# Optimization experiments

Measured on AMD Instinct MI355X. Metric: run time of the kernel, lower is better.

Reference implementation:

```python
import jax, jax.numpy as jnp
import numpy as np

N_NODES = 50000
N_EDGES = 800000
N_GRAPHS = 8
BN_EPS = 1e-5


def setup_inputs() -> dict:
    key = jax.random.key(0)
    ks = iter(jax.random.split(key, 40))
    d = {}
    d["x"] = jax.random.normal(next(ks), (N_NODES, 3), dtype=jnp.float32)
    d["edge_index"] = jax.random.randint(next(ks), (2, N_EDGES), 0, N_NODES, dtype=jnp.int32)
    d["batch"] = jnp.sort(jax.random.randint(next(ks), (N_NODES,), 0, N_GRAPHS, dtype=jnp.int32))
    conv_in = [3, 64, 128]  # dense concat widths feeding each GCN layer
    for i, cin in enumerate(conv_in):
        d[f"W{i}"] = jax.random.normal(next(ks), (cin, 64), dtype=jnp.float32) * (1.0 / np.sqrt(cin))
        d[f"b{i}"] = jax.random.normal(next(ks), (64,), dtype=jnp.float32) * 0.05
        d[f"g{i}"] = jax.random.uniform(next(ks), (64,), dtype=jnp.float32) + 0.5
        d[f"beta{i}"] = jax.random.normal(next(ks), (64,), dtype=jnp.float32) * 0.05
        d[f"rm{i}"] = jax.random.normal(next(ks), (64,), dtype=jnp.float32) * 0.05
        d[f"rv{i}"] = jax.random.uniform(next(ks), (64,), dtype=jnp.float32) + 0.5
    def lin(k, i, o):
        return (jax.random.normal(k, (i, o), dtype=jnp.float32) * (1.0 / np.sqrt(i)),)
    d["enc_w0"], = lin(next(ks), 256, 128); d["enc_b0"] = jax.random.normal(next(ks), (128,), jnp.float32) * 0.05
    d["enc_w1"], = lin(next(ks), 128, 64); d["enc_b1"] = jax.random.normal(next(ks), (64,), jnp.float32) * 0.05
    d["dec_w0"], = lin(next(ks), 64, 32); d["dec_b0"] = jax.random.normal(next(ks), (32,), jnp.float32) * 0.05
    d["dec_w1"], = lin(next(ks), 32, 1); d["dec_b1"] = jax.random.normal(next(ks), (1,), jnp.float32) * 0.05
    return d


def reference(x, edge_index, batch,
              W0, b0, g0, beta0, rm0, rv0,
              W1, b1, g1, beta1, rm1, rv1,
              W2, b2, g2, beta2, rm2, rv2,
              enc_w0, enc_b0, enc_w1, enc_b1,
              dec_w0, dec_b0, dec_w1, dec_b1):
    N = x.shape[0]
    loops = jnp.arange(N, dtype=edge_index.dtype)
    src = jnp.concatenate([edge_index[0], loops])  # GCNConv adds self loops
    dst = jnp.concatenate([edge_index[1], loops])
    deg = jax.ops.segment_sum(jnp.ones_like(src, dtype=x.dtype), dst, num_segments=N)
    dinv = jnp.where(deg > 0, jax.lax.rsqrt(deg), 0.0)
    coef = (dinv[src] * dinv[dst])[:, None]  # symmetric normalization per edge

    def conv_bn_relu(h, W, b, g, beta, rm, rv):
        hw = h @ W                                    # [N, 64]
        out = jax.ops.segment_sum(hw[src] * coef, dst, num_segments=N) + b
        out = (out - rm) * (g * jax.lax.rsqrt(rv + BN_EPS)) + beta  # BN eval mode
        return jax.nn.relu(out)

    params = [(W0, b0, g0, beta0, rm0, rv0),
              (W1, b1, g1, beta1, rm1, rv1),
              (W2, b2, g2, beta2, rm2, rv2)]
    prev = []
    h = x
    for p in params:  # dense connectivity: concat all previous concat-outputs
        h = conv_bn_relu(h, *p)
        h = jnp.concatenate(prev + [h], axis=1)
        prev.append(h)

    e = jax.nn.relu(jax.nn.relu(h @ enc_w0 + enc_b0) @ enc_w1 + enc_b1)  # [N, 64]
    counts = jax.ops.segment_sum(jnp.ones((N,), x.dtype), batch, num_segments=N_GRAPHS)
    gfeat = jax.ops.segment_sum(e, batch, num_segments=N_GRAPHS) / jnp.maximum(counts, 1.0)[:, None]
    out = jax.nn.relu(gfeat @ dec_w0 + dec_b0) @ dec_w1 + dec_b1  # [G, 1]
    return out[:, 0]  # torch.squeeze(output, 1) since num_classes == 1
```

## Files before the change

kernel.cpp:

```cpp
#include <hip/hip_runtime.h>
#include <hip/hip_fp16.h>

#define NN 50000
#define NE 800000
#define NG 8
#define BN_EPS 1e-5f
#define NBLK ((NN + 255) / 256)
#define NPART 8
#define HLD 192

typedef __attribute__((ext_vector_type(8))) short bf16x8;
typedef __attribute__((ext_vector_type(4))) float f32x4;

static __device__ __forceinline__ unsigned short f2bf(float f) {
    unsigned int u = __float_as_uint(f);
    unsigned int r = (u + 0x7FFFu + ((u >> 16) & 1u)) >> 16;
    return (unsigned short)r;
}
static __device__ __forceinline__ float bf2f(unsigned short h) {
    return __uint_as_float((unsigned int)h << 16);
}


static __device__ __forceinline__ void pack_one(const float* W, int NOUT, int li,
                                                float v_override, bool use_override,
                                                unsigned short* ph, unsigned short* pl) {
    int j = li & 7;
    int lane = (li >> 3) & 63;
    int rest = li >> 9;
    int NF = NOUT >> 4;
    int f = rest % NF, ks = rest / NF;
    int k = ks * 32 + (lane >> 4) * 8 + j;
    int col = f * 16 + (lane & 15);
    float v = use_override ? v_override : W[k * NOUT + col];
    unsigned short hi = f2bf(v);
    ph[li] = hi;
    pl[li] = f2bf(v - bf2f(hi));
}

__global__ __launch_bounds__(256) void pack_all(
        const float* __restrict__ W1, const float* __restrict__ W2,
        const float* __restrict__ We0, const float* __restrict__ We1,
        unsigned short* __restrict__ Wp1h, unsigned short* __restrict__ Wp1l,
        unsigned short* __restrict__ Wp2h, unsigned short* __restrict__ Wp2l,
        unsigned short* __restrict__ We0h, unsigned short* __restrict__ We0l,
        unsigned short* __restrict__ We1h, unsigned short* __restrict__ We1l,
        int* __restrict__ degi, float* __restrict__ gfeat_part) {
    int idx = blockIdx.x * 256 + threadIdx.x;
    if (idx < NN) degi[idx] = 0;
    if (idx < NPART * NG * 64) gfeat_part[idx] = 0.0f;
    if (idx < 4096) {
        pack_one(W1, 64, idx, 0.f, false, Wp1h, Wp1l);
    } else if (idx < 12288) {
        pack_one(W2, 64, idx - 4096, 0.f, false, Wp2h, Wp2l);
    } else if (idx < 36864) {
        int li = idx - 12288;
        int j = li & 7;
        int lane = (li >> 3) & 63;
        int rest = li >> 9;
        int f = rest % 8, ks = rest / 8;
        int k = ks * 32 + (lane >> 4) * 8 + j;
        int col = f * 16 + (lane & 15);
        float v = (k < 64) ? (We0[k * 128 + col] + We0[(k + 64) * 128 + col])
                           : We0[(k + 64) * 128 + col];
        pack_one(nullptr, 128, li, v, true, We0h, We0l);
    } else if (idx < 45056) {
        pack_one(We1, 64, idx - 36864, 0.f, false, We1h, We1l);
    }
}


__global__ __launch_bounds__(256) void count_deg(const int4* __restrict__ dst4,
                                                 int* __restrict__ degi) {
    int t = blockIdx.x * 256 + threadIdx.x;
    if (t < NE / 4) {
        int4 d = dst4[t];
        atomicAdd(&degi[d.x], 1);
        atomicAdd(&degi[d.y], 1);
        atomicAdd(&degi[d.z], 1);
        atomicAdd(&degi[d.w], 1);
    }
}

__global__ __launch_bounds__(256) void scan_partial(const int* __restrict__ degi,
                                                    const float* __restrict__ x,
                                                    int* __restrict__ rowptr,
                                                    int* __restrict__ bsum,
                                                    float* __restrict__ dinv,
                                                    float* __restrict__ xs) {
    __shared__ int sh[256];
    const int tid = threadIdx.x;
    const int i = blockIdx.x * 256 + tid;
    int v = (i < NN) ? degi[i] : 0;
    if (i < NN) {
        float di = rsqrtf((float)(v + 1));
        dinv[i] = di;
        xs[i * 3 + 0] = x[i * 3 + 0] * di;
        xs[i * 3 + 1] = x[i * 3 + 1] * di;
        xs[i * 3 + 2] = x[i * 3 + 2] * di;
    }
    sh[tid] = v;
    __syncthreads();
#pragma unroll
    for (int off = 1; off < 256; off <<= 1) {
        int t = (tid >= off) ? sh[tid - off] : 0;
        __syncthreads();
        sh[tid] += t;
        __syncthreads();
    }
    if (i < NN) rowptr[i] = sh[tid] - v;
    if (tid == 255) bsum[blockIdx.x] = sh[255];
}

__global__ __launch_bounds__(256) void scan_finalize(const int* __restrict__ bsum,
                                                     int* __restrict__ rowptr,
                                                     int* __restrict__ cursor) {
    __shared__ int sh[256];
    const int tid = threadIdx.x;
    int v = (tid < NBLK) ? bsum[tid] : 0;
    sh[tid] = v;
    __syncthreads();
#pragma unroll
    for (int off = 1; off < 256; off <<= 1) {
        int t = (tid >= off) ? sh[tid - off] : 0;
        __syncthreads();
        sh[tid] += t;
        __syncthreads();
    }
    const int base = (blockIdx.x == 0) ? 0 : sh[blockIdx.x - 1];
    const int i = blockIdx.x * 256 + tid;
    if (i < NN) {
        int r = rowptr[i] + base;
        rowptr[i] = r;
        cursor[i] = r;
    }
    if (i == 0) rowptr[NN] = NE;
}

__global__ __launch_bounds__(256) void fill_csr(const int* __restrict__ src,
                                                const int* __restrict__ dst,
                                                int* __restrict__ cursor,
                                                unsigned short* __restrict__ esrc16) {
    int e = blockIdx.x * 256 + threadIdx.x;
    if (e < NE) {
        int s = src[e], d = dst[e];
        int p = atomicAdd(&cursor[d], 1);
        esrc16[p] = (unsigned short)s;
    }
}


__global__ __launch_bounds__(256) void agg_l0(
        const float* __restrict__ xs,
        const int* __restrict__ rowptr,
        const unsigned short* __restrict__ esrc16,
        const float* __restrict__ dinv,
        const float* __restrict__ W0, const float* __restrict__ b,
        const float* __restrict__ g, const float* __restrict__ beta,
        const float* __restrict__ rm, const float* __restrict__ rv,
        unsigned short* __restrict__ Hhi, unsigned short* __restrict__ Hlo) {
    const int wid = (blockIdx.x * 256 + threadIdx.x) >> 6;
    const int lane = threadIdx.x & 63;
    if (wid >= NN) return;
    const int beg = rowptr[wid], end = rowptr[wid + 1];
    float a0 = 0.0f, a1 = 0.0f, a2 = 0.0f;
    for (int e = beg + lane; e < end; e += 64) {
        int s = esrc16[e];
        a0 += xs[s * 3 + 0];
        a1 += xs[s * 3 + 1];
        a2 += xs[s * 3 + 2];
    }
#pragma unroll
    for (int off = 32; off >= 1; off >>= 1) {
        a0 += __shfl_xor(a0, off, 64);
        a1 += __shfl_xor(a1, off, 64);
        a2 += __shfl_xor(a2, off, 64);
    }
    a0 += xs[wid * 3 + 0];
    a1 += xs[wid * 3 + 1];
    a2 += xs[wid * 3 + 2];
    const float di = dinv[wid];
    a0 *= di; a1 *= di; a2 *= di;
    const int ch = lane;
    float v = a0 * W0[ch] + a1 * W0[64 + ch] + a2 * W0[128 + ch] + b[ch];
    float sc = g[ch] * rsqrtf(rv[ch] + BN_EPS);
    v = (v - rm[ch]) * sc + beta[ch];
    v = fmaxf(v, 0.0f);
    unsigned short hi = f2bf(v);
    Hhi[(size_t)wid * HLD + ch] = hi;
    Hlo[(size_t)wid * HLD + ch] = f2bf(v - bf2f(hi));
}


template<int K>
__global__ __launch_bounds__(256, 2) void mfma_tab(
        const unsigned short* __restrict__ Ahi,
        const unsigned short* __restrict__ Alo, int lda,
        const unsigned short* __restrict__ Bph,
        const unsigned short* __restrict__ Bpl,
        const float* __restrict__ dinv,
        __half* __restrict__ outH) {
    constexpr int KS = K / 32;
    const int wave = threadIdx.x >> 6;
    const int lane = threadIdx.x & 63;
    const int rbase = blockIdx.x * 64 + wave * 16;
    int arow = rbase + (lane & 15);
    if (arow >= NN) arow = NN - 1;
    const int kbase = (lane >> 4) * 8;

    bf16x8 bh[KS][4], bl[KS][4];
#pragma unroll
    for (int ks = 0; ks < KS; ks++)
#pragma unroll
        for (int f = 0; f < 4; f++) {
            bh[ks][f] = *reinterpret_cast<const bf16x8*>(Bph + (size_t)((ks * 4 + f) * 64 + lane) * 8);
            bl[ks][f] = *reinterpret_cast<const bf16x8*>(Bpl + (size_t)((ks * 4 + f) * 64 + lane) * 8);
        }

    const unsigned short* pa_hi = Ahi + (size_t)arow * lda + kbase;
    const unsigned short* pa_lo = Alo + (size_t)arow * lda + kbase;
    bf16x8 ah[KS], al[KS];
#pragma unroll
    for (int ks = 0; ks < KS; ks++) {
        ah[ks] = *reinterpret_cast<const bf16x8*>(pa_hi + ks * 32);
        al[ks] = *reinterpret_cast<const bf16x8*>(pa_lo + ks * 32);
    }

    f32x4 acc[4];
#pragma unroll
    for (int f = 0; f < 4; f++) acc[f] = (f32x4){0.f, 0.f, 0.f, 0.f};

#pragma unroll
    for (int ks = 0; ks < KS; ks++)
#pragma unroll
        for (int f = 0; f < 4; f++) {
            acc[f] = __builtin_amdgcn_mfma_f32_16x16x32_bf16(ah[ks], bh[ks][f], acc[f], 0, 0, 0);
            acc[f] = __builtin_amdgcn_mfma_f32_16x16x32_bf16(ah[ks], bl[ks][f], acc[f], 0, 0, 0);
            acc[f] = __builtin_amdgcn_mfma_f32_16x16x32_bf16(al[ks], bh[ks][f], acc[f], 0, 0, 0);
        }

    const int drow0 = rbase + (lane >> 4) * 4;
    const int dcol = lane & 15;
#pragma unroll
    for (int f = 0; f < 4; f++) {
#pragma unroll
        for (int r = 0; r < 4; r++) {
            int row = drow0 + r;
            if (row < NN)
                outH[(size_t)row * 64 + f * 16 + dcol] = __float2half(acc[f][r] * dinv[row]);
        }
    }
}


__global__ __launch_bounds__(256, 2) void enc_fused(
        const unsigned short* __restrict__ Hhi,
        const unsigned short* __restrict__ Hlo,
        const unsigned short* __restrict__ We0h, const unsigned short* __restrict__ We0l,
        const float* __restrict__ b0,
        const unsigned short* __restrict__ We1h, const unsigned short* __restrict__ We1l,
        const float* __restrict__ b1,
        const int* __restrict__ batch,
        float* __restrict__ gfeat_part) {
    __shared__ float ldsT[4][16][133];
    __shared__ float poolw[4][64];
    __shared__ float pool[NG][64];
    const int tid = threadIdx.x;
    const int wave = tid >> 6;
    const int lane = tid & 63;
    const int rbase = blockIdx.x * 64 + wave * 16;

    int arow = rbase + (lane & 15);
    if (arow >= NN) arow = NN - 1;
    const int kbase = (lane >> 4) * 8;
    f32x4 acc[8];
#pragma unroll
    for (int f = 0; f < 8; f++) acc[f] = (f32x4){0.f, 0.f, 0.f, 0.f};

    const unsigned short* pa_hi = Hhi + (size_t)arow * HLD + kbase;
    const unsigned short* pa_lo = Hlo + (size_t)arow * HLD + kbase;

    bf16x8 cbh[8], cbl[8], nbh[8], nbl[8];
#pragma unroll
    for (int f = 0; f < 8; f++) {
        cbh[f] = *reinterpret_cast<const bf16x8*>(We0h + (size_t)(f * 64 + lane) * 8);
        cbl[f] = *reinterpret_cast<const bf16x8*>(We0l + (size_t)(f * 64 + lane) * 8);
    }
#pragma unroll
    for (int ks = 0; ks < 6; ks++) {
        if (ks < 5) {
#pragma unroll
            for (int f = 0; f < 8; f++) {
                nbh[f] = *reinterpret_cast<const bf16x8*>(We0h + (size_t)(((ks + 1) * 8 + f) * 64 + lane) * 8);
                nbl[f] = *reinterpret_cast<const bf16x8*>(We0l + (size_t)(((ks + 1) * 8 + f) * 64 + lane) * 8);
            }
        }
        bf16x8 ah = *reinterpret_cast<const bf16x8*>(pa_hi + ks * 32);
        bf16x8 al = *reinterpret_cast<const bf16x8*>(pa_lo + ks * 32);
#pragma unroll
        for (int f = 0; f < 8; f++) {
            acc[f] = __builtin_amdgcn_mfma_f32_16x16x32_bf16(ah, cbh[f], acc[f], 0, 0, 0);
            acc[f] = __builtin_amdgcn_mfma_f32_16x16x32_bf16(ah, cbl[f], acc[f], 0, 0, 0);
            acc[f] = __builtin_amdgcn_mfma_f32_16x16x32_bf16(al, cbh[f], acc[f], 0, 0, 0);
        }
        if (ks < 5) {
#pragma unroll
            for (int f = 0; f < 8; f++) { cbh[f] = nbh[f]; cbl[f] = nbl[f]; }
        }
    }

    const int lrow0 = (lane >> 4) * 4;
    const int dcol = lane & 15;
#pragma unroll
    for (int f = 0; f < 8; f++) {
#pragma unroll
        for (int r = 0; r < 4; r++) {
            float v = fmaxf(acc[f][r] + b0[f * 16 + dcol], 0.0f);
            ldsT[wave][lrow0 + r][f * 16 + dcol] = v;
        }
    }
    __syncthreads();

    bf16x8 wbh[4][4], wbl[4][4];
#pragma unroll
    for (int ks = 0; ks < 4; ks++)
#pragma unroll
        for (int f = 0; f < 4; f++) {
            wbh[ks][f] = *reinterpret_cast<const bf16x8*>(We1h + (size_t)((ks * 4 + f) * 64 + lane) * 8);
            wbl[ks][f] = *reinterpret_cast<const bf16x8*>(We1l + (size_t)((ks * 4 + f) * 64 + lane) * 8);
        }

    f32x4 acc2[4];
#pragma unroll
    for (int f = 0; f < 4; f++) acc2[f] = (f32x4){0.f, 0.f, 0.f, 0.f};

    const int trow = lane & 15;
#pragma unroll
    for (int ks = 0; ks < 4; ks++) {
        bf16x8 ah, al;
#pragma unroll
        for (int j = 0; j < 8; j++) {
            float tv = ldsT[wave][trow][ks * 32 + (lane >> 4) * 8 + j];
            unsigned short hi = f2bf(tv);
            ah[j] = (short)hi;
            al[j] = (short)f2bf(tv - bf2f(hi));
        }
#pragma unroll
        for (int f = 0; f < 4; f++) {
            acc2[f] = __builtin_amdgcn_mfma_f32_16x16x32_bf16(ah, wbh[ks][f], acc2[f], 0, 0, 0);
            acc2[f] = __builtin_amdgcn_mfma_f32_16x16x32_bf16(ah, wbl[ks][f], acc2[f], 0, 0, 0);
            acc2[f] = __builtin_amdgcn_mfma_f32_16x16x32_bf16(al, wbh[ks][f], acc2[f], 0, 0, 0);
        }
    }

    float vout[4][4];
#pragma unroll
    for (int f = 0; f < 4; f++)
#pragma unroll
        for (int r = 0; r < 4; r++) {
            int row = rbase + lrow0 + r;
            vout[f][r] = (row < NN) ? fmaxf(acc2[f][r] + b1[f * 16 + dcol], 0.0f) : 0.0f;
        }

    const int blk_row0 = blockIdx.x * 64;
    const int blk_rowN = min(blk_row0 + 63, NN - 1);
    const int g0 = batch[blk_row0];
    const int p = blockIdx.x & (NPART - 1);

    if (g0 == batch[blk_rowN]) {
#pragma unroll
        for (int f = 0; f < 4; f++) {
            float s = (vout[f][0] + vout[f][1]) + (vout[f][2] + vout[f][3]);
            s += __shfl_xor(s, 16, 64);
            s += __shfl_xor(s, 32, 64);
            if ((lane >> 4) == 0) poolw[wave][f * 16 + dcol] = s;
        }
        __syncthreads();
        if (tid < 64) {
            float s = (poolw[0][tid] + poolw[1][tid]) + (poolw[2][tid] + poolw[3][tid]);
            atomicAdd(&gfeat_part[(p * NG + g0) * 64 + tid], s);
        }
    } else {
        for (int i = tid; i < NG * 64; i += 256) ((float*)pool)[i] = 0.0f;
        __syncthreads();
#pragma unroll
        for (int r = 0; r < 4; r++) {
            int row = rbase + lrow0 + r;
            if (row < NN) {
                int g = batch[row];
#pragma unroll
                for (int f = 0; f < 4; f++)
                    atomicAdd(&pool[g][f * 16 + dcol], vout[f][r]);
            }
        }
        __syncthreads();
        for (int i = tid; i < NG * 64; i += 256) {
            float s = ((float*)pool)[i];
            if (s != 0.0f) atomicAdd(&gfeat_part[p * NG * 64 + i], s);
        }
    }
}


__global__ __launch_bounds__(256) void gather_bn_relu(
        const __half2* __restrict__ tab2,
        const int* __restrict__ rowptr,
        const unsigned short* __restrict__ esrc16,
        const float* __restrict__ dinv,
        const float* __restrict__ b, const float* __restrict__ g,
        const float* __restrict__ beta, const float* __restrict__ rm,
        const float* __restrict__ rv,
        unsigned short* __restrict__ Hhi, unsigned short* __restrict__ Hlo, int cbase) {
    const int wid = (blockIdx.x * 256 + threadIdx.x) >> 6;
    const int lane = threadIdx.x & 63;
    const int c2 = lane & 31;
    const int grp = lane >> 5;
    if (wid >= NN) return;
    const int beg = rowptr[wid], end = rowptr[wid + 1];
    float a0 = 0.0f, a1 = 0.0f;
    int e = beg + grp;
    for (; e + 14 < end; e += 16) {
        int s0 = esrc16[e],      s1 = esrc16[e + 2],  s2 = esrc16[e + 4],  s3 = esrc16[e + 6];
        int s4 = esrc16[e + 8],  s5 = esrc16[e + 10], s6 = esrc16[e + 12], s7 = esrc16[e + 14];
        float2 f0 = __half22float2(tab2[(size_t)s0 * 32 + c2]);
        float2 f1 = __half22float2(tab2[(size_t)s1 * 32 + c2]);
        float2 f2 = __half22float2(tab2[(size_t)s2 * 32 + c2]);
        float2 f3 = __half22float2(tab2[(size_t)s3 * 32 + c2]);
        float2 f4 = __half22float2(tab2[(size_t)s4 * 32 + c2]);
        float2 f5 = __half22float2(tab2[(size_t)s5 * 32 + c2]);
        float2 f6 = __half22float2(tab2[(size_t)s6 * 32 + c2]);
        float2 f7 = __half22float2(tab2[(size_t)s7 * 32 + c2]);
        a0 += ((f0.x + f1.x) + (f2.x + f3.x)) + ((f4.x + f5.x) + (f6.x + f7.x));
        a1 += ((f0.y + f1.y) + (f2.y + f3.y)) + ((f4.y + f5.y) + (f6.y + f7.y));
    }
    for (; e + 6 < end; e += 8) {
        int s0 = esrc16[e], s1 = esrc16[e + 2], s2 = esrc16[e + 4], s3 = esrc16[e + 6];
        float2 f0 = __half22float2(tab2[(size_t)s0 * 32 + c2]);
        float2 f1 = __half22float2(tab2[(size_t)s1 * 32 + c2]);
        float2 f2 = __half22float2(tab2[(size_t)s2 * 32 + c2]);
        float2 f3 = __half22float2(tab2[(size_t)s3 * 32 + c2]);
        a0 += (f0.x + f1.x) + (f2.x + f3.x);
        a1 += (f0.y + f1.y) + (f2.y + f3.y);
    }
    for (; e < end; e += 2) {
        float2 f = __half22float2(tab2[(size_t)esrc16[e] * 32 + c2]);
        a0 += f.x;
        a1 += f.y;
    }
    a0 += __shfl_xor(a0, 32, 64);
    a1 += __shfl_xor(a1, 32, 64);
    float2 fs = __half22float2(tab2[(size_t)wid * 32 + c2]);
    a0 += fs.x;
    a1 += fs.y;
    const float di = dinv[wid];
    a0 *= di;
    a1 *= di;
    const int ch0 = 2 * c2, ch1 = 2 * c2 + 1;
    float v0 = (a0 + b[ch0] - rm[ch0]) * (g[ch0] * rsqrtf(rv[ch0] + BN_EPS)) + beta[ch0];
    float v1 = (a1 + b[ch1] - rm[ch1]) * (g[ch1] * rsqrtf(rv[ch1] + BN_EPS)) + beta[ch1];
    v0 = fmaxf(v0, 0.0f);
    v1 = fmaxf(v1, 0.0f);
    if (grp == 0) {
        unsigned short h0 = f2bf(v0), h1 = f2bf(v1);
        unsigned short l0 = f2bf(v0 - bf2f(h0)), l1 = f2bf(v1 - bf2f(h1));
        size_t o = (size_t)wid * HLD + cbase + ch0;
        *reinterpret_cast<unsigned int*>(&Hhi[o]) = (unsigned int)h0 | ((unsigned int)h1 << 16);
        *reinterpret_cast<unsigned int*>(&Hlo[o]) = (unsigned int)l0 | ((unsigned int)l1 << 16);
    }
}


__global__ __launch_bounds__(256) void dec_kernel(
        const float* __restrict__ gfeat_part, const int* __restrict__ batch,
        const float* __restrict__ w0, const float* __restrict__ b0,
        const float* __restrict__ w1, const float* __restrict__ b1,
        float* __restrict__ out) {
    __shared__ float mg[NG][64];
    __shared__ float mc[NG];
    __shared__ float t1[NG][32];
    const int tid = threadIdx.x;
    for (int idx = tid; idx < NG * 64; idx += 256) {
        float s = 0.0f;
#pragma unroll
        for (int p = 0; p < NPART; p++) s += gfeat_part[p * NG * 64 + idx];
        mg[idx >> 6][idx & 63] = s;
    }
    if (tid < NG) {
        int lo = 0, hi = NN;
        while (lo < hi) { int m = (lo + hi) >> 1; if (batch[m] < tid) lo = m + 1; else hi = m; }
        int s0 = lo;
        lo = 0; hi = NN;
        while (lo < hi) { int m = (lo + hi) >> 1; if (batch[m] < tid + 1) lo = m + 1; else hi = m; }
        mc[tid] = (float)(lo - s0);
    }
    __syncthreads();
    const int g = tid >> 5, c = tid & 31;
    float inv = 1.0f / fmaxf(mc[g], 1.0f);
    float acc = b0[c];
    for (int k = 0; k < 64; k++)
        acc = fmaf(mg[g][k] * inv, w0[k * 32 + c], acc);
    t1[g][c] = fmaxf(acc, 0.0f);
    __syncthreads();
    if (tid < NG) {
        float o = b1[0];
        for (int c2 = 0; c2 < 32; c2++) o = fmaf(t1[tid][c2], w1[c2], o);
        out[tid] = o;
    }
}


extern "C" void kernel_launch(void* const* d_in, const int* in_sizes, int n_in,
                              void* d_out, int out_size, void* d_ws, size_t ws_size,
                              hipStream_t stream) {
    const float* x      = (const float*)d_in[0];
    const int*   ei     = (const int*)d_in[1];
    const int*   batch  = (const int*)d_in[2];
    const float* W0     = (const float*)d_in[3];
    const float* b0     = (const float*)d_in[4];
    const float* g0     = (const float*)d_in[5];
    const float* beta0  = (const float*)d_in[6];
    const float* rm0    = (const float*)d_in[7];
    const float* rv0    = (const float*)d_in[8];
    const float* W1     = (const float*)d_in[9];
    const float* b1     = (const float*)d_in[10];
    const float* g1     = (const float*)d_in[11];
    const float* beta1  = (const float*)d_in[12];
    const float* rm1    = (const float*)d_in[13];
    const float* rv1    = (const float*)d_in[14];
    const float* W2     = (const float*)d_in[15];
    const float* b2     = (const float*)d_in[16];
    const float* g2     = (const float*)d_in[17];
    const float* beta2  = (const float*)d_in[18];
    const float* rm2    = (const float*)d_in[19];
    const float* rv2    = (const float*)d_in[20];
    const float* enc_w0 = (const float*)d_in[21];
    const float* enc_b0 = (const float*)d_in[22];
    const float* enc_w1 = (const float*)d_in[23];
    const float* enc_b1 = (const float*)d_in[24];
    const float* dec_w0 = (const float*)d_in[25];
    const float* dec_b0 = (const float*)d_in[26];
    const float* dec_w1 = (const float*)d_in[27];
    const float* dec_b1 = (const float*)d_in[28];

    const int* esrc = ei;
    const int* edst = ei + NE;

    char* wsb = (char*)d_ws;
    unsigned short* Hhi = (unsigned short*)wsb;
    unsigned short* Hlo = Hhi + (size_t)NN * HLD;
    int*   degi   = (int*)(Hlo + (size_t)NN * HLD);
    int*   rowptr = degi + NN;
    int*   cursor = rowptr + NN + 1;
    unsigned short* esrc16 = (unsigned short*)(cursor + NN);
    __half* tabh  = (__half*)(esrc16 + NE);
    float* dinv   = (float*)(tabh + (size_t)NN * 64);
    float* xs     = dinv + NN;
    float* gfeat_part = xs + (size_t)NN * 3;
    int*   bsum   = (int*)(gfeat_part + NPART * NG * 64);
    unsigned short* wp = (unsigned short*)(bsum + NBLK);
    unsigned short* Wp1h = wp;              unsigned short* Wp1l = Wp1h + 64 * 64;
    unsigned short* Wp2h = Wp1l + 64 * 64;  unsigned short* Wp2l = Wp2h + 128 * 64;
    unsigned short* We0h = Wp2l + 128 * 64; unsigned short* We0l = We0h + 192 * 128;
    unsigned short* We1h = We0l + 192 * 128;unsigned short* We1l = We1h + 128 * 64;

    const int GRID_MFMA = (NN + 63) / 64;
    const int GRID_64   = (NN * 64 + 255) / 256;

    pack_all<<<NBLK, 256, 0, stream>>>(W1, W2, enc_w0, enc_w1,
                                       Wp1h, Wp1l, Wp2h, Wp2l,
                                       We0h, We0l, We1h, We1l, degi, gfeat_part);

    count_deg<<<(NE / 4 + 255) / 256, 256, 0, stream>>>((const int4*)edst, degi);
    scan_partial<<<NBLK, 256, 0, stream>>>(degi, x, rowptr, bsum, dinv, xs);
    scan_finalize<<<NBLK, 256, 0, stream>>>(bsum, rowptr, cursor);
    fill_csr<<<(NE + 255) / 256, 256, 0, stream>>>(esrc, edst, cursor, esrc16);

    agg_l0<<<GRID_64, 256, 0, stream>>>(xs, rowptr, esrc16, dinv,
                                        W0, b0, g0, beta0, rm0, rv0, Hhi, Hlo);

    mfma_tab<64><<<GRID_MFMA, 256, 0, stream>>>(Hhi, Hlo, HLD, Wp1h, Wp1l, dinv, tabh);
    gather_bn_relu<<<GRID_64, 256, 0, stream>>>((const __half2*)tabh, rowptr, esrc16, dinv,
                                                b1, g1, beta1, rm1, rv1, Hhi, Hlo, 64);

    mfma_tab<128><<<GRID_MFMA, 256, 0, stream>>>(Hhi, Hlo, HLD, Wp2h, Wp2l, dinv, tabh);
    gather_bn_relu<<<GRID_64, 256, 0, stream>>>((const __half2*)tabh, rowptr, esrc16, dinv,
                                                b2, g2, beta2, rm2, rv2, Hhi, Hlo, 128);

    enc_fused<<<GRID_MFMA, 256, 0, stream>>>(Hhi, Hlo, We0h, We0l, enc_b0,
                                             We1h, We1l, enc_b1, batch, gfeat_part);

    dec_kernel<<<1, 256, 0, stream>>>(gfeat_part, batch, dec_w0, dec_b0, dec_w1, dec_b1, (float*)d_out);
}
```

Baseline: 230.5 us.

## Partition degree counting and CSR fill by destination range across blocks

Degree counting and CSR fill now run 8 blocks per 2048-edge chunk. Each block handles only the destinations in one eighth of the node range, so the atomics issued by a block land in a smaller address region. This is meant to improve L2 locality, for example keeping each partition's atomics within one XCD's cache, and to reduce atomic contention spread. The cost is that every edge's dst is read 8 times and most threads do no work after the range check.

```diff
diff --git a/kernel.cpp b/kernel.cpp
--- a/kernel.cpp
+++ b/kernel.cpp
@@ -8,6 +8,9 @@
 #define NBLK ((NN + 255) / 256)
 #define NPART 8
 #define HLD 192
+#define FC_CHUNK 2048
+#define FC_NCHUNK ((NE + FC_CHUNK - 1) / FC_CHUNK)
+#define PART_SZ (NN / 8)
 
 typedef __attribute__((ext_vector_type(8))) short bf16x8;
 typedef __attribute__((ext_vector_type(4))) float f32x4;
@@ -70,17 +73,37 @@
 }
 
 
-__global__ __launch_bounds__(256) void count_deg(const int4* __restrict__ dst4,
-                                                 int* __restrict__ degi) {
-    int t = blockIdx.x * 256 + threadIdx.x;
-    if (t < NE / 4) {
-        int4 d = dst4[t];
-        atomicAdd(&degi[d.x], 1);
-        atomicAdd(&degi[d.y], 1);
-        atomicAdd(&degi[d.z], 1);
-        atomicAdd(&degi[d.w], 1);
-    }
-}
+__global__ __launch_bounds__(256) void count_deg_p(const int* __restrict__ dst,
+                                                   int* __restrict__ degi) {
+    const int part = blockIdx.x & 7;
+    const int chunk = blockIdx.x >> 3;
+    const int lo = part * PART_SZ, hi = lo + PART_SZ;
+    const int e0 = chunk * FC_CHUNK;
+    const int e1 = min(e0 + FC_CHUNK, NE);
+    for (int e = e0 + threadIdx.x; e < e1; e += 256) {
+        int d = dst[e];
+        if (d >= lo && d < hi) atomicAdd(&degi[d], 1);
+    }
+}
+
+__global__ __launch_bounds__(256) void fill_csr_p(const int* __restrict__ src,
+                                                  const int* __restrict__ dst,
+                                                  int* __restrict__ cursor,
+                                                  unsigned short* __restrict__ esrc16) {
+    const int part = blockIdx.x & 7;
+    const int chunk = blockIdx.x >> 3;
+    const int lo = part * PART_SZ, hi = lo + PART_SZ;
+    const int e0 = chunk * FC_CHUNK;
+    const int e1 = min(e0 + FC_CHUNK, NE);
+    for (int e = e0 + threadIdx.x; e < e1; e += 256) {
+        int d = dst[e];
+        if (d >= lo && d < hi) {
+            int p = atomicAdd(&cursor[d], 1);
+            esrc16[p] = (unsigned short)src[e];
+        }
+    }
+}
+
 
 __global__ __launch_bounds__(256) void scan_partial(const int* __restrict__ degi,
                                                     const float* __restrict__ x,
@@ -135,18 +158,6 @@
         cursor[i] = r;
     }
     if (i == 0) rowptr[NN] = NE;
-}
-
-__global__ __launch_bounds__(256) void fill_csr(const int* __restrict__ src,
-                                                const int* __restrict__ dst,
-                                                int* __restrict__ cursor,
-                                                unsigned short* __restrict__ esrc16) {
-    int e = blockIdx.x * 256 + threadIdx.x;
-    if (e < NE) {
-        int s = src[e], d = dst[e];
-        int p = atomicAdd(&cursor[d], 1);
-        esrc16[p] = (unsigned short)s;
-    }
 }
 
 
@@ -565,15 +576,16 @@
 
     const int GRID_MFMA = (NN + 63) / 64;
     const int GRID_64   = (NN * 64 + 255) / 256;
+    const int GRID_PART = 8 * FC_NCHUNK;
 
     pack_all<<<NBLK, 256, 0, stream>>>(W1, W2, enc_w0, enc_w1,
                                        Wp1h, Wp1l, Wp2h, Wp2l,
                                        We0h, We0l, We1h, We1l, degi, gfeat_part);
 
-    count_deg<<<(NE / 4 + 255) / 256, 256, 0, stream>>>((const int4*)edst, degi);
+    count_deg_p<<<GRID_PART, 256, 0, stream>>>(edst, degi);
     scan_partial<<<NBLK, 256, 0, stream>>>(degi, x, rowptr, bsum, dinv, xs);
     scan_finalize<<<NBLK, 256, 0, stream>>>(bsum, rowptr, cursor);
-    fill_csr<<<(NE + 255) / 256, 256, 0, stream>>>(esrc, edst, cursor, esrc16);
+    fill_csr_p<<<GRID_PART, 256, 0, stream>>>(esrc, edst, cursor, esrc16);
 
     agg_l0<<<GRID_64, 256, 0, stream>>>(xs, rowptr, esrc16, dinv,
                                         W0, b0, g0, beta0, rm0, rv0, Hhi, Hlo);
```

Result: no change. 227.7 us (-1.2%).
